# Kernel optimization log

Hardware: AMD Instinct MI355X
Metric: run time of the kernel (lower is better)

Reference implementation:

```python
import jax, jax.numpy as jnp
import numpy as np


def setup_inputs() -> dict:
    key = jax.random.key(0)
    k1, k2, k3, k4 = jax.random.split(key, 4)
    B, Q, K, H, D = 2, 2048, 2048, 16, 64
    qs = jax.random.normal(k1, (B, Q, H, D), dtype=jnp.float32)
    ks = jax.random.normal(k2, (B, K, H, D), dtype=jnp.float32)
    vs = jax.random.normal(k3, (B, K, H, D), dtype=jnp.float32)
    # valid lengths in [1, K] so no row is fully masked
    valid_lens = jnp.maximum(jax.random.randint(k4, (B,), 0, K + 1, dtype=jnp.int32), 1)
    return {"qs": qs, "ks": ks, "vs": vs, "valid_lens": valid_lens}


def reference(qs, ks, vs, valid_lens):
    # Faithful math of ScanAttention: scaled dot-product attention with a
    # per-batch key-validity mask (online-softmax scan == exact softmax).
    B, Q, H, D = qs.shape
    K = ks.shape[1]
    scale = 1.0 / jnp.sqrt(jnp.float32(D))
    # [B, H, Q, K]
    scores = jnp.einsum('bqhd,bkhd->bhqk', qs * scale, ks)
    ks_mask = jnp.arange(K)[None, :] < valid_lens[:, None]  # [B, K]
    scores = jnp.where(ks_mask[:, None, None, :], scores, -jnp.inf)
    attn = jax.nn.softmax(scores, axis=-1)
    out = jnp.einsum('bhqk,bkhd->bqhd', attn, vs)  # [B, Q, H, D]
    return out
```

## Files before the change

kernel.cpp:

```cpp
#include <hip/hip_runtime.h>
#include <hip/hip_bf16.h>

typedef __bf16 bf16t;
typedef bf16t bf16x8 __attribute__((ext_vector_type(8)));
typedef float f32x4 __attribute__((ext_vector_type(4)));
typedef unsigned short u16x4 __attribute__((ext_vector_type(4)));
typedef unsigned short u16x8 __attribute__((ext_vector_type(8)));

#define NB 2
#define NQ 2048
#define NK 2048
#define NH 16
#define ND 64
#define HD (NH * ND)
#define QBLK 64
#define KVBLK 64
#define SCALE_LOG2E 0.18033688011112042f

__global__ __launch_bounds__(256)
void scan_attn(const float* __restrict__ qs, const float* __restrict__ ks,
               const float* __restrict__ vs, const int* __restrict__ vlen,
               float* __restrict__ out)
{
    const int bid  = blockIdx.x;
    const int b    = bid & 1;
    const int h    = (bid >> 1) & 15;
    const int qt   = bid >> 5;
    const int tid  = threadIdx.x;
    const int wid  = tid >> 6;
    const int lane = tid & 63;
    const int g    = lane >> 4;
    const int ql   = lane & 15;
    const int swq  = (ql & 7) << 4;
    const int q    = qt * QBLK + wid * 16 + ql;

    const int nkv    = vlen[b];
    const int ntiles = (nkv + KVBLK - 1) >> 6;
    const int rem    = nkv & 63;

    const float* qptr = qs + ((size_t)b * NQ + q) * HD + h * ND;
    const float* kptr = ks + (size_t)b * NK * HD + h * ND;
    const float* vptr = vs + (size_t)b * NK * HD + h * ND;

    __shared__ __align__(16) char k_lds[2][KVBLK * 64 * 2];
    __shared__ __align__(16) char vt_lds[2][64 * KVBLK * 2];
    __shared__ __align__(16) unsigned short plds[4][16][72];

    bf16x8 qf[2];
#pragma unroll
    for (int c = 0; c < 2; ++c) {
        const float* p = qptr + 32 * c + 8 * g;
        f32x4 lo = *reinterpret_cast<const f32x4*>(p);
        f32x4 hi = *reinterpret_cast<const f32x4*>(p + 4);
#pragma unroll
        for (int j = 0; j < 4; ++j) {
            qf[c][j]     = (bf16t)(lo[j] * SCALE_LOG2E);
            qf[c][4 + j] = (bf16t)(hi[j] * SCALE_LOG2E);
        }
    }

    const int skr  = tid >> 2;
    const int skc  = (tid & 3) << 4;
    const int skc2 = skc * 2;
    const int ksw  = (skr & 7) << 4;
    const int svd  = tid & 63;
    const int svk  = (tid >> 6) << 4;
    const int svk2 = svk * 2;
    const int vsw  = (svd & 7) << 4;

    f32x4 kreg[4];
    float vreg[16];

    auto load_tile = [&](int kb) {
        const float* kp = kptr + (size_t)(kb + skr) * HD + skc;
#pragma unroll
        for (int i = 0; i < 4; ++i)
            kreg[i] = *reinterpret_cast<const f32x4*>(kp + 4 * i);
        const float* vp = vptr + (size_t)(kb + svk) * HD + svd;
#pragma unroll
        for (int j = 0; j < 16; ++j)
            vreg[j] = vp[(size_t)j * HD];
    };

    auto store_tile = [&](int buf) {
        u16x8 w0, w1;
#pragma unroll
        for (int i = 0; i < 4; ++i)
#pragma unroll
            for (int j = 0; j < 4; ++j) {
                const int e = 4 * i + j;
                const unsigned short u =
                    __builtin_bit_cast(unsigned short, (bf16t)kreg[i][j]);
                if (e < 8) w0[e] = u; else w1[e - 8] = u;
            }
        char* kb_ = k_lds[buf] + skr * 128;
        *reinterpret_cast<u16x8*>(kb_ + (skc2 ^ ksw))        = w0;
        *reinterpret_cast<u16x8*>(kb_ + ((skc2 + 16) ^ ksw)) = w1;

        u16x8 x0, x1;
#pragma unroll
        for (int j = 0; j < 16; ++j) {
            const unsigned short u =
                __builtin_bit_cast(unsigned short, (bf16t)vreg[j]);
            if (j < 8) x0[j] = u; else x1[j - 8] = u;
        }
        char* vb_ = vt_lds[buf] + svd * 128;
        *reinterpret_cast<u16x8*>(vb_ + (svk2 ^ vsw))        = x0;
        *reinterpret_cast<u16x8*>(vb_ + ((svk2 + 16) ^ vsw)) = x1;
    };

    float mrun = -__builtin_inff();
    float lrun = 0.0f;
    f32x4 o[4];
#pragma unroll
    for (int n = 0; n < 4; ++n) o[n] = (f32x4){0.f, 0.f, 0.f, 0.f};

    load_tile(0);
    store_tile(0);
    __syncthreads();

    int cur = 0;
    for (int t = 0; t < ntiles; ++t) {
        const int kb = t << 6;
        const bool has_next = (t + 1) < ntiles;
        if (has_next) load_tile(kb + KVBLK);

        const char* kbuf = k_lds[cur];
        f32x4 s[4];
#pragma unroll
        for (int m2 = 0; m2 < 4; ++m2) {
            f32x4 acc = (f32x4){0.f, 0.f, 0.f, 0.f};
            const char* krow = kbuf + (16 * m2 + ql) * 128;
#pragma unroll
            for (int c = 0; c < 2; ++c) {
                bf16x8 kf = *reinterpret_cast<const bf16x8*>(
                    krow + ((64 * c + 16 * g) ^ swq));
                acc = __builtin_amdgcn_mfma_f32_16x16x32_bf16(kf, qf[c], acc, 0, 0, 0);
            }
            s[m2] = acc;
        }

        if (rem && t == ntiles - 1) {
            const int krem = nkv - kb;
#pragma unroll
            for (int m2 = 0; m2 < 4; ++m2)
#pragma unroll
                for (int r = 0; r < 4; ++r)
                    if (16 * m2 + 4 * g + r >= krem) s[m2][r] = -__builtin_inff();
        }

        float pmax = -__builtin_inff();
#pragma unroll
        for (int m2 = 0; m2 < 4; ++m2)
#pragma unroll
            for (int r = 0; r < 4; ++r) pmax = fmaxf(pmax, s[m2][r]);
        pmax = fmaxf(pmax, __shfl_xor(pmax, 16));
        pmax = fmaxf(pmax, __shfl_xor(pmax, 32));
        const float mnew  = fmaxf(mrun, pmax);
        const float alpha = exp2f(mrun - mnew);

        float ps = 0.0f;
#pragma unroll
        for (int m2 = 0; m2 < 4; ++m2) {
            u16x4 pk;
#pragma unroll
            for (int r = 0; r < 4; ++r) {
                float pv = exp2f(s[m2][r] - mnew);
                bf16t pb = (bf16t)pv;
                ps += (float)pb;
                pk[r] = __builtin_bit_cast(unsigned short, pb);
            }
            *reinterpret_cast<u16x4*>(&plds[wid][ql][16 * m2 + 4 * g]) = pk;
        }
        ps += __shfl_xor(ps, 16);
        ps += __shfl_xor(ps, 32);
        lrun = lrun * alpha + ps;
        mrun = mnew;
#pragma unroll
        for (int n = 0; n < 4; ++n)
#pragma unroll
            for (int r = 0; r < 4; ++r) o[n][r] *= alpha;

        const char* vbuf = vt_lds[cur];
#pragma unroll
        for (int kc = 0; kc < 2; ++kc) {
            bf16x8 pf = __builtin_bit_cast(bf16x8,
                *reinterpret_cast<const u16x8*>(&plds[wid][ql][32 * kc + 8 * g]));
#pragma unroll
            for (int n = 0; n < 4; ++n) {
                bf16x8 vf = *reinterpret_cast<const bf16x8*>(
                    vbuf + (16 * n + ql) * 128 + ((64 * kc + 16 * g) ^ swq));
                o[n] = __builtin_amdgcn_mfma_f32_16x16x32_bf16(vf, pf, o[n], 0, 0, 0);
            }
        }

        if (has_next) store_tile(cur ^ 1);
        __syncthreads();
        cur ^= 1;
    }

    const float inv = 1.0f / lrun;
    float* op = out + ((size_t)b * NQ + q) * HD + h * ND;
#pragma unroll
    for (int n = 0; n < 4; ++n)
#pragma unroll
        for (int r = 0; r < 4; ++r)
            op[16 * n + 4 * g + r] = o[n][r] * inv;
}

extern "C" void kernel_launch(void* const* d_in, const int* in_sizes, int n_in,
                              void* d_out, int out_size, void* d_ws, size_t ws_size,
                              hipStream_t stream)
{
    const float* qs   = (const float*)d_in[0];
    const float* ks   = (const float*)d_in[1];
    const float* vs   = (const float*)d_in[2];
    const int*   vlen = (const int*)d_in[3];
    float* out = (float*)d_out;

    dim3 grid(NB * NH * (NQ / QBLK));
    dim3 block(256);
    scan_attn<<<grid, block, 0, stream>>>(qs, ks, vs, vlen, out);
}
```

Baseline: 72.47 us.

## Switch attention to 32x32 MFMA with in-register P and lazy rescaling

Moves both QK^T and PV to 32x32x16 bf16 MFMA, so each wave covers 32 queries and each block 128 queries, halving the grid. The P matrix is now repacked in registers with packed bf16 conversion and permlane32 swaps, replacing the LDS round trip. Online-softmax rescaling is skipped unless the new max exceeds the running max by a threshold, which removes most exp and multiply work on the output accumulators. The trade-offs are fewer blocks (512) and therefore possibly lower occupancy, higher register pressure, and the use of unnormalized P values that can grow up to 2^8 before rescaling.

```diff
diff --git a/kernel.cpp b/kernel.cpp
--- a/kernel.cpp
+++ b/kernel.cpp
@@ -4,8 +4,9 @@
 typedef __bf16 bf16t;
 typedef bf16t bf16x8 __attribute__((ext_vector_type(8)));
 typedef float f32x4 __attribute__((ext_vector_type(4)));
-typedef unsigned short u16x4 __attribute__((ext_vector_type(4)));
+typedef float f32x16 __attribute__((ext_vector_type(16)));
 typedef unsigned short u16x8 __attribute__((ext_vector_type(8)));
+typedef unsigned int u32x4 __attribute__((ext_vector_type(4)));
 
 #define NB 2
 #define NQ 2048
@@ -13,9 +14,29 @@
 #define NH 16
 #define ND 64
 #define HD (NH * ND)
-#define QBLK 64
 #define KVBLK 64
 #define SCALE_LOG2E 0.18033688011112042f
+#define RESCALE_THR 8.0f
+
+__device__ inline unsigned cvt_pk_bf16(float a, float b) {
+    unsigned r;
+    asm("v_cvt_pk_bf16_f32 %0, %1, %2" : "=v"(r) : "v"(a), "v"(b));
+    return r;
+}
+
+__device__ inline void plswap(unsigned& a, unsigned& b) {
+#if __has_builtin(__builtin_amdgcn_permlane32_swap)
+    auto r = __builtin_amdgcn_permlane32_swap(a, b, false, false);
+    a = r[0]; b = r[1];
+#else
+    const unsigned as = __shfl_xor((int)a, 32);
+    const unsigned bs = __shfl_xor((int)b, 32);
+    const bool hi = (threadIdx.x & 32) != 0;
+    const unsigned na = hi ? bs : a;
+    const unsigned nb = hi ? b : as;
+    a = na; b = nb;
+#endif
+}
 
 __global__ __launch_bounds__(256)
 void scan_attn(const float* __restrict__ qs, const float* __restrict__ ks,
@@ -29,10 +50,10 @@
     const int tid  = threadIdx.x;
     const int wid  = tid >> 6;
     const int lane = tid & 63;
-    const int g    = lane >> 4;
-    const int ql   = lane & 15;
+    const int ql   = lane & 31;
+    const int hi   = lane >> 5;
     const int swq  = (ql & 7) << 4;
-    const int q    = qt * QBLK + wid * 16 + ql;
+    const int q    = qt * 128 + wid * 32 + ql;
 
     const int nkv    = vlen[b];
     const int ntiles = (nkv + KVBLK - 1) >> 6;
@@ -44,39 +65,36 @@
 
     __shared__ __align__(16) char k_lds[2][KVBLK * 64 * 2];
     __shared__ __align__(16) char vt_lds[2][64 * KVBLK * 2];
-    __shared__ __align__(16) unsigned short plds[4][16][72];
-
-    bf16x8 qf[2];
-#pragma unroll
-    for (int c = 0; c < 2; ++c) {
-        const float* p = qptr + 32 * c + 8 * g;
+
+    bf16x8 qf[4];
+#pragma unroll
+    for (int c = 0; c < 4; ++c) {
+        const float* p = qptr + 16 * c + 8 * hi;
         f32x4 lo = *reinterpret_cast<const f32x4*>(p);
-        f32x4 hi = *reinterpret_cast<const f32x4*>(p + 4);
+        f32x4 h4 = *reinterpret_cast<const f32x4*>(p + 4);
 #pragma unroll
         for (int j = 0; j < 4; ++j) {
             qf[c][j]     = (bf16t)(lo[j] * SCALE_LOG2E);
-            qf[c][4 + j] = (bf16t)(hi[j] * SCALE_LOG2E);
+            qf[c][4 + j] = (bf16t)(h4[j] * SCALE_LOG2E);
         }
     }
 
     const int skr  = tid >> 2;
-    const int skc  = (tid & 3) << 4;
-    const int skc2 = skc * 2;
+    const int skc2 = (tid & 3) << 5;
     const int ksw  = (skr & 7) << 4;
     const int svd  = tid & 63;
-    const int svk  = (tid >> 6) << 4;
-    const int svk2 = svk * 2;
+    const int svk2 = (tid >> 6) << 5;
     const int vsw  = (svd & 7) << 4;
 
     f32x4 kreg[4];
     float vreg[16];
 
     auto load_tile = [&](int kb) {
-        const float* kp = kptr + (size_t)(kb + skr) * HD + skc;
+        const float* kp = kptr + (size_t)(kb + skr) * HD + ((tid & 3) << 4);
 #pragma unroll
         for (int i = 0; i < 4; ++i)
             kreg[i] = *reinterpret_cast<const f32x4*>(kp + 4 * i);
-        const float* vp = vptr + (size_t)(kb + svk) * HD + svd;
+        const float* vp = vptr + (size_t)(kb + ((tid >> 6) << 4)) * HD + svd;
 #pragma unroll
         for (int j = 0; j < 16; ++j)
             vreg[j] = vp[(size_t)j * HD];
@@ -111,9 +129,7 @@
 
     float mrun = -__builtin_inff();
     float lrun = 0.0f;
-    f32x4 o[4];
-#pragma unroll
-    for (int n = 0; n < 4; ++n) o[n] = (f32x4){0.f, 0.f, 0.f, 0.f};
+    f32x16 o[2] = {};
 
     load_tile(0);
     store_tile(0);
@@ -126,71 +142,80 @@
         if (has_next) load_tile(kb + KVBLK);
 
         const char* kbuf = k_lds[cur];
-        f32x4 s[4];
-#pragma unroll
-        for (int m2 = 0; m2 < 4; ++m2) {
-            f32x4 acc = (f32x4){0.f, 0.f, 0.f, 0.f};
-            const char* krow = kbuf + (16 * m2 + ql) * 128;
-#pragma unroll
-            for (int c = 0; c < 2; ++c) {
+        f32x16 s[2];
+#pragma unroll
+        for (int h2 = 0; h2 < 2; ++h2) {
+            f32x16 acc = {};
+            const char* krow = kbuf + (32 * h2 + ql) * 128;
+#pragma unroll
+            for (int c = 0; c < 4; ++c) {
                 bf16x8 kf = *reinterpret_cast<const bf16x8*>(
-                    krow + ((64 * c + 16 * g) ^ swq));
-                acc = __builtin_amdgcn_mfma_f32_16x16x32_bf16(kf, qf[c], acc, 0, 0, 0);
-            }
-            s[m2] = acc;
+                    krow + ((32 * c + 16 * hi) ^ swq));
+                acc = __builtin_amdgcn_mfma_f32_32x32x16_bf16(kf, qf[c], acc, 0, 0, 0);
+            }
+            s[h2] = acc;
         }
 
         if (rem && t == ntiles - 1) {
             const int krem = nkv - kb;
 #pragma unroll
-            for (int m2 = 0; m2 < 4; ++m2)
-#pragma unroll
-                for (int r = 0; r < 4; ++r)
-                    if (16 * m2 + 4 * g + r >= krem) s[m2][r] = -__builtin_inff();
+            for (int h2 = 0; h2 < 2; ++h2)
+#pragma unroll
+                for (int r = 0; r < 16; ++r)
+                    if (32 * h2 + (r & 3) + 8 * (r >> 2) + 4 * hi >= krem)
+                        s[h2][r] = -__builtin_inff();
         }
 
         float pmax = -__builtin_inff();
 #pragma unroll
-        for (int m2 = 0; m2 < 4; ++m2)
-#pragma unroll
-            for (int r = 0; r < 4; ++r) pmax = fmaxf(pmax, s[m2][r]);
-        pmax = fmaxf(pmax, __shfl_xor(pmax, 16));
+        for (int h2 = 0; h2 < 2; ++h2)
+#pragma unroll
+            for (int r = 0; r < 16; ++r) pmax = fmaxf(pmax, s[h2][r]);
         pmax = fmaxf(pmax, __shfl_xor(pmax, 32));
-        const float mnew  = fmaxf(mrun, pmax);
-        const float alpha = exp2f(mrun - mnew);
+
+        if (!__all(pmax <= mrun + RESCALE_THR)) {
+            const float mnew  = fmaxf(mrun, pmax);
+            const float alpha = exp2f(mrun - mnew);
+            lrun *= alpha;
+            o[0] *= alpha;
+            o[1] *= alpha;
+            mrun = mnew;
+        }
 
         float ps = 0.0f;
 #pragma unroll
-        for (int m2 = 0; m2 < 4; ++m2) {
-            u16x4 pk;
-#pragma unroll
-            for (int r = 0; r < 4; ++r) {
-                float pv = exp2f(s[m2][r] - mnew);
-                bf16t pb = (bf16t)pv;
-                ps += (float)pb;
-                pk[r] = __builtin_bit_cast(unsigned short, pb);
-            }
-            *reinterpret_cast<u16x4*>(&plds[wid][ql][16 * m2 + 4 * g]) = pk;
-        }
-        ps += __shfl_xor(ps, 16);
+        for (int h2 = 0; h2 < 2; ++h2)
+#pragma unroll
+            for (int r = 0; r < 16; ++r) {
+                const float pv = exp2f(s[h2][r] - mrun);
+                s[h2][r] = pv;
+                ps += pv;
+            }
         ps += __shfl_xor(ps, 32);
-        lrun = lrun * alpha + ps;
-        mrun = mnew;
-#pragma unroll
-        for (int n = 0; n < 4; ++n)
-#pragma unroll
-            for (int r = 0; r < 4; ++r) o[n][r] *= alpha;
+        lrun += ps;
+
+        bf16x8 pf[4];
+#pragma unroll
+        for (int c = 0; c < 4; ++c) {
+            const int h2 = c >> 1, r0 = (c & 1) * 8;
+            unsigned a0 = cvt_pk_bf16(s[h2][r0 + 0], s[h2][r0 + 1]);
+            unsigned b0 = cvt_pk_bf16(s[h2][r0 + 4], s[h2][r0 + 5]);
+            plswap(a0, b0);
+            unsigned a1 = cvt_pk_bf16(s[h2][r0 + 2], s[h2][r0 + 3]);
+            unsigned b1 = cvt_pk_bf16(s[h2][r0 + 6], s[h2][r0 + 7]);
+            plswap(a1, b1);
+            pf[c] = __builtin_bit_cast(bf16x8, (u32x4){a0, a1, b0, b1});
+        }
 
         const char* vbuf = vt_lds[cur];
 #pragma unroll
-        for (int kc = 0; kc < 2; ++kc) {
-            bf16x8 pf = __builtin_bit_cast(bf16x8,
-                *reinterpret_cast<const u16x8*>(&plds[wid][ql][32 * kc + 8 * g]));
-#pragma unroll
-            for (int n = 0; n < 4; ++n) {
+        for (int dt = 0; dt < 2; ++dt) {
+            const char* vrow = vbuf + (32 * dt + ql) * 128;
+#pragma unroll
+            for (int c = 0; c < 4; ++c) {
                 bf16x8 vf = *reinterpret_cast<const bf16x8*>(
-                    vbuf + (16 * n + ql) * 128 + ((64 * kc + 16 * g) ^ swq));
-                o[n] = __builtin_amdgcn_mfma_f32_16x16x32_bf16(vf, pf, o[n], 0, 0, 0);
+                    vrow + ((32 * c + 16 * hi) ^ swq));
+                o[dt] = __builtin_amdgcn_mfma_f32_32x32x16_bf16(vf, pf[c], o[dt], 0, 0, 0);
             }
         }
 
@@ -202,10 +227,14 @@
     const float inv = 1.0f / lrun;
     float* op = out + ((size_t)b * NQ + q) * HD + h * ND;
 #pragma unroll
-    for (int n = 0; n < 4; ++n)
-#pragma unroll
-        for (int r = 0; r < 4; ++r)
-            op[16 * n + 4 * g + r] = o[n][r] * inv;
+    for (int dt = 0; dt < 2; ++dt)
+#pragma unroll
+        for (int rg = 0; rg < 4; ++rg) {
+            f32x4 w;
+#pragma unroll
+            for (int e = 0; e < 4; ++e) w[e] = o[dt][4 * rg + e] * inv;
+            *reinterpret_cast<f32x4*>(op + 32 * dt + 8 * rg + 4 * hi) = w;
+        }
 }
 
 extern "C" void kernel_launch(void* const* d_in, const int* in_sizes, int n_in,
@@ -218,7 +247,7 @@
     const int*   vlen = (const int*)d_in[3];
     float* out = (float*)d_out;
 
-    dim3 grid(NB * NH * (NQ / QBLK));
+    dim3 grid(NB * NH * (NQ / 128));
     dim3 block(256);
     scan_attn<<<grid, block, 0, stream>>>(qs, ks, vs, vlen, out);
 }
```

Result: faster. 61.44 us (-15.2%).
